# Kernel tuning notes

Measured on AMD Instinct MI355X. Metric: run time of the kernel, lower is better.

The kernel has to match this reference:

```python
import jax, jax.numpy as jnp
import numpy as np

D = 4096      # model dim
H = 32        # query heads (== kv heads; GQA path in source is buggy, default is MHA)
HD = D // H   # head_dim = 128
BASE = 10000.0


def _rope_cos_sin(S):
    # inv_freq over half the head dim, duplicated to full head_dim (standard RoPE)
    inv_freq = 1.0 / (BASE ** (jnp.arange(0, HD, 2, dtype=jnp.float32) / HD))
    t = jnp.arange(S, dtype=jnp.float32)
    freqs = jnp.outer(t, inv_freq)                      # [S, HD//2]
    cos = jnp.concatenate([jnp.cos(freqs)] * 2, axis=-1)  # [S, HD]
    sin = jnp.concatenate([jnp.sin(freqs)] * 2, axis=-1)
    return cos[None, None], sin[None, None]             # [1,1,S,HD]


def _rotate_half(x):
    x1, x2 = jnp.split(x, 2, axis=-1)
    return jnp.concatenate((-x2, x1), axis=-1)


def setup_inputs() -> dict:
    key = jax.random.key(0)
    ks = jax.random.split(key, 5)
    B, S = 2, 2048
    x = jax.random.normal(ks[0], (B, S, D), dtype=jnp.float32)
    # causal mask: 1 = attend, 0 = masked
    mask = jnp.tril(jnp.ones((S, S), dtype=bool))[None, None]  # [1,1,S,S]
    w = lambda k: jax.random.normal(k, (D, D), dtype=jnp.float32) * 0.02
    return {"x": x, "mask": mask, "Wq": w(ks[1]), "Wk": w(ks[2]), "Wv": w(ks[3]), "Wo": w(ks[4])}


def reference(x, mask, Wq, Wk, Wv, Wo):
    B, S, _ = x.shape
    scale = HD ** -0.5
    # torch nn.Linear: y = x @ W.T
    q = (x @ Wq.T).reshape(B, S, H, HD).transpose(0, 2, 1, 3)  # [B,H,S,HD]
    k = (x @ Wk.T).reshape(B, S, H, HD).transpose(0, 2, 1, 3)
    v = (x @ Wv.T).reshape(B, S, H, HD).transpose(0, 2, 1, 3)
    cos, sin = _rope_cos_sin(S)
    q = q * cos + _rotate_half(q) * sin
    k = k * cos + _rotate_half(k) * sin
    scores = jnp.einsum('bhqd,bhkd->bhqk', q, k) * scale       # [B,H,S,S]
    scores = jnp.where(mask, scores, jnp.float32(-10000.0))
    probs = jax.nn.softmax(scores, axis=-1)                    # dropout p=0.0
    ctx = jnp.einsum('bhqk,bhkd->bhqd', probs, v)
    ctx = ctx.transpose(0, 2, 1, 3).reshape(B, S, H * HD)      # [B,S,D]
    return ctx @ Wo.T
```

## Files before the change

kernel.cpp:

```cpp
#include <hip/hip_runtime.h>

typedef __bf16 bf16x8 __attribute__((ext_vector_type(8)));
typedef float  f32x4  __attribute__((ext_vector_type(4)));
typedef unsigned short ushort8v __attribute__((ext_vector_type(8)));

#define DEV __device__ __forceinline__

constexpr int Dm = 4096;
constexpr int Sq = 2048;
constexpr int Bb = 2;
constexpr int Hh = 32;
constexpr int HDd = 128;

DEV unsigned short f2bf(float f) {
  union { float f; unsigned u; } v; v.f = f;
  unsigned u = v.u;
  return (unsigned short)((u + 0x7fffu + ((u >> 16) & 1u)) >> 16);
}
DEV float bf2f(unsigned short s) {
  union { unsigned u; float f; } v; v.u = ((unsigned)s) << 16;
  return v.f;
}

__global__ __launch_bounds__(256) void cast_f32_bf16(const float* __restrict__ src,
                                                     unsigned short* __restrict__ dst,
                                                     int n8) {
  int i = blockIdx.x * 256 + threadIdx.x;
  if (i >= n8) return;
  const float4* s4 = (const float4*)src;
  float4 a = s4[2 * i], b = s4[2 * i + 1];
  ushort8v o;
  o[0] = f2bf(a.x); o[1] = f2bf(a.y); o[2] = f2bf(a.z); o[3] = f2bf(a.w);
  o[4] = f2bf(b.x); o[5] = f2bf(b.y); o[6] = f2bf(b.z); o[7] = f2bf(b.w);
  *(ushort8v*)(dst + 8 * i) = o;
}

__global__ __launch_bounds__(256) void rope_tables(float* __restrict__ cosT,
                                                   float* __restrict__ sinT) {
  int idx = blockIdx.x * 256 + threadIdx.x;
  int s = idx >> 6, i = idx & 63;
  float inv = expf(-(float)i * (9.210340371976184f / 64.0f));
  float f = (float)s * inv;
  cosT[idx] = cosf(f);
  sinT[idx] = sinf(f);
}

template <int WF32>
__global__ __launch_bounds__(256) void gemm_nt(const unsigned short* __restrict__ A,
                                               const unsigned short* __restrict__ Bw,
                                               unsigned short* __restrict__ Cb,
                                               float* __restrict__ Cf, int K) {
  constexpr int TM = 128, BK = 64;
  __shared__ unsigned short lA[TM * BK];
  __shared__ unsigned short lB[TM * BK];
  const int tid = threadIdx.x;
  const int l = tid & 63, w = tid >> 6;
  const int wm = (w >> 1) * 64, wn = (w & 1) * 64;
  const int m0 = blockIdx.x * TM, n0 = blockIdx.y * TM;
  f32x4 acc[4][4] = {};

  const int scb = (tid & 7) * 16;
  const unsigned short* Ag = A + (size_t)m0 * K;
  const unsigned short* Bg = Bw + (size_t)n0 * K;

  for (int k0 = 0; k0 < K; k0 += BK) {
    __syncthreads();
#pragma unroll
    for (int i = 0; i < 4; i++) {
      int row = (tid >> 3) + 32 * i;
      uint4 va = *(const uint4*)((const char*)Ag + ((size_t)row * K + k0) * 2 + scb);
      uint4 vb = *(const uint4*)((const char*)Bg + ((size_t)row * K + k0) * 2 + scb);
      int lo = row * 128 + (scb ^ ((row & 7) << 4));
      *(uint4*)((char*)lA + lo) = va;
      *(uint4*)((char*)lB + lo) = vb;
    }
    __syncthreads();
#pragma unroll
    for (int kc = 0; kc < 2; kc++) {
      bf16x8 af[4], bfr[4];
#pragma unroll
      for (int mi = 0; mi < 4; mi++) {
        int row = wm + mi * 16 + (l & 15);
        int cb = (kc * 64 + (l >> 4) * 16) ^ ((row & 7) << 4);
        af[mi] = *(const bf16x8*)((const char*)lA + row * 128 + cb);
      }
#pragma unroll
      for (int ni = 0; ni < 4; ni++) {
        int row = wn + ni * 16 + (l & 15);
        int cb = (kc * 64 + (l >> 4) * 16) ^ ((row & 7) << 4);
        bfr[ni] = *(const bf16x8*)((const char*)lB + row * 128 + cb);
      }
#pragma unroll
      for (int mi = 0; mi < 4; mi++)
#pragma unroll
        for (int ni = 0; ni < 4; ni++)
          acc[mi][ni] = __builtin_amdgcn_mfma_f32_16x16x32_bf16(af[mi], bfr[ni], acc[mi][ni], 0, 0, 0);
    }
  }
#pragma unroll
  for (int mi = 0; mi < 4; mi++) {
    int mrow = m0 + wm + mi * 16 + (l >> 4) * 4;
#pragma unroll
    for (int ni = 0; ni < 4; ni++) {
      int ncol = n0 + wn + ni * 16 + (l & 15);
#pragma unroll
      for (int r = 0; r < 4; r++) {
        if constexpr (WF32)
          Cf[(size_t)(mrow + r) * Dm + ncol] = acc[mi][ni][r];
        else
          Cb[(size_t)(mrow + r) * Dm + ncol] = f2bf(acc[mi][ni][r]);
      }
    }
  }
}

__global__ __launch_bounds__(256) void rope_apply(unsigned short* __restrict__ Q,
                                                  unsigned short* __restrict__ Kt,
                                                  const float* __restrict__ cosT,
                                                  const float* __restrict__ sinT) {
  int idx = blockIdx.x * 256 + threadIdx.x;
  unsigned short* P = blockIdx.y ? Kt : Q;
  int j = idx & 7;
  int h = (idx >> 3) & 31;
  int m = idx >> 8;
  int s = m & (Sq - 1);
  size_t base = (size_t)m * Dm + h * HDd + j * 8;
  ushort8v u1 = *(ushort8v*)(P + base);
  ushort8v u2 = *(ushort8v*)(P + base + 64);
  const float* cp = cosT + s * 64 + j * 8;
  const float* sp = sinT + s * 64 + j * 8;
  ushort8v o1, o2;
#pragma unroll
  for (int e = 0; e < 8; e++) {
    float c = cp[e], sn = sp[e];
    float x1 = bf2f(u1[e]), x2 = bf2f(u2[e]);
    o1[e] = f2bf(x1 * c - x2 * sn);
    o2[e] = f2bf(x2 * c + x1 * sn);
  }
  *(ushort8v*)(P + base) = o1;
  *(ushort8v*)(P + base + 64) = o2;
}

__global__ __launch_bounds__(256) void transpose_v(const unsigned short* __restrict__ V,
                                                   unsigned short* __restrict__ VT) {
  __shared__ unsigned short t[32][33];
  int bh = blockIdx.z;
  int s0 = blockIdx.x * 32, d0 = blockIdx.y * 32;
  int tx = threadIdx.x, ty = threadIdx.y;
  int b = bh >> 5, h = bh & 31;
#pragma unroll
  for (int i = 0; i < 4; i++) {
    int row = ty + i * 8;
    t[row][tx] = V[((size_t)(b * Sq + s0 + row)) * Dm + h * HDd + d0 + tx];
  }
  __syncthreads();
#pragma unroll
  for (int i = 0; i < 4; i++) {
    int row = ty + i * 8;
    VT[((size_t)bh * HDd + d0 + row) * Sq + s0 + tx] = t[tx][row];
  }
}

__global__ __launch_bounds__(256) void flash_attn(const unsigned short* __restrict__ Qg,
                                                  const unsigned short* __restrict__ Kg,
                                                  const unsigned short* __restrict__ VTg,
                                                  unsigned short* __restrict__ Ctx) {
  constexpr int QB = 64, KVB = 64, PP = 88;
  __shared__ unsigned short lK[KVB * HDd];
  __shared__ unsigned short lV[HDd * KVB];
  __shared__ unsigned short lP[4][16 * PP];
  const int tid = threadIdx.x, l = tid & 63, w = tid >> 6;
  const int q0 = blockIdx.x * QB;
  const int bh = blockIdx.y, b = bh >> 5, h = bh & 31;

  bf16x8 qf[4];
  {
    int qrow = q0 + w * 16 + (l & 15);
    const unsigned short* qp = Qg + ((size_t)(b * Sq + qrow)) * Dm + h * HDd + (l >> 4) * 8;
#pragma unroll
    for (int c = 0; c < 4; c++) qf[c] = *(const bf16x8*)(qp + c * 32);
  }

  f32x4 acc[8] = {};
  float mrun[4] = {-1e30f, -1e30f, -1e30f, -1e30f};
  float lrun[4] = {0.f, 0.f, 0.f, 0.f};
  const float scale = 0.08838834764831845f;
  const float L2E = 1.4426950408889634f;

  const int ntile = blockIdx.x + 1;
  for (int t = 0; t < ntile; t++) {
    int kv0 = t * KVB;
    __syncthreads();
#pragma unroll
    for (int i = 0; i < 4; i++) {
      int c = tid + 256 * i;
      int row = c >> 4, cb = (c & 15) * 16;
      uint4 vd = *(const uint4*)((const char*)Kg +
                                 (((size_t)(b * Sq + kv0 + row)) * Dm + h * HDd) * 2 + cb);
      *(uint4*)((char*)lK + row * 256 + (cb ^ ((row & 7) << 4))) = vd;
    }
#pragma unroll
    for (int i = 0; i < 4; i++) {
      int c = tid + 256 * i;
      int row = c >> 3, cb = (c & 7) * 16;
      uint4 vd = *(const uint4*)((const char*)VTg +
                                 (((size_t)(bh * HDd + row)) * Sq + kv0) * 2 + cb);
      *(uint4*)((char*)lV + row * 128 + (cb ^ ((row & 7) << 4))) = vd;
    }
    __syncthreads();

    f32x4 sc[4] = {};
#pragma unroll
    for (int nb = 0; nb < 4; nb++) {
      int kvr = nb * 16 + (l & 15);
#pragma unroll
      for (int c = 0; c < 4; c++) {
        int cb = (c * 64 + (l >> 4) * 16) ^ ((kvr & 7) << 4);
        bf16x8 kf = *(const bf16x8*)((const char*)lK + kvr * 256 + cb);
        sc[nb] = __builtin_amdgcn_mfma_f32_16x16x32_bf16(qf[c], kf, sc[nb], 0, 0, 0);
      }
    }

    float sv[4][4];
#pragma unroll
    for (int nb = 0; nb < 4; nb++) {
      int kvg = kv0 + nb * 16 + (l & 15);
#pragma unroll
      for (int r = 0; r < 4; r++) {
        int qg = q0 + w * 16 + (l >> 4) * 4 + r;
        float vv = sc[nb][r] * scale;
        sv[nb][r] = (kvg <= qg) ? vv : -1e30f;
      }
    }
    float rmax[4];
#pragma unroll
    for (int r = 0; r < 4; r++)
      rmax[r] = fmaxf(fmaxf(sv[0][r], sv[1][r]), fmaxf(sv[2][r], sv[3][r]));
#pragma unroll
    for (int d = 1; d < 16; d <<= 1)
#pragma unroll
      for (int r = 0; r < 4; r++) rmax[r] = fmaxf(rmax[r], __shfl_xor(rmax[r], d, 64));

    float mnew[4], alpha[4], psum[4];
#pragma unroll
    for (int r = 0; r < 4; r++) {
      mnew[r] = fmaxf(mrun[r], rmax[r]);
      alpha[r] = exp2f((mrun[r] - mnew[r]) * L2E);
      psum[r] = 0.f;
    }
    float pvv[4][4];
#pragma unroll
    for (int nb = 0; nb < 4; nb++)
#pragma unroll
      for (int r = 0; r < 4; r++) {
        float pe = exp2f((sv[nb][r] - mnew[r]) * L2E);
        pvv[nb][r] = pe;
        psum[r] += pe;
      }
#pragma unroll
    for (int d = 1; d < 16; d <<= 1)
#pragma unroll
      for (int r = 0; r < 4; r++) psum[r] += __shfl_xor(psum[r], d, 64);
#pragma unroll
    for (int r = 0; r < 4; r++) {
      lrun[r] = lrun[r] * alpha[r] + psum[r];
      mrun[r] = mnew[r];
    }
#pragma unroll
    for (int hdnb = 0; hdnb < 8; hdnb++)
#pragma unroll
      for (int r = 0; r < 4; r++) acc[hdnb][r] *= alpha[r];

    unsigned short* P = lP[w];
#pragma unroll
    for (int nb = 0; nb < 4; nb++)
#pragma unroll
      for (int r = 0; r < 4; r++)
        P[((l >> 4) * 4 + r) * PP + nb * 16 + (l & 15)] = f2bf(pvv[nb][r]);

    bf16x8 pf[2];
#pragma unroll
    for (int kc = 0; kc < 2; kc++)
      pf[kc] = *(const bf16x8*)(P + (l & 15) * PP + kc * 32 + (l >> 4) * 8);
#pragma unroll
    for (int hdnb = 0; hdnb < 8; hdnb++) {
      int hdr = hdnb * 16 + (l & 15);
#pragma unroll
      for (int kc = 0; kc < 2; kc++) {
        int cb = (kc * 64 + (l >> 4) * 16) ^ ((hdr & 7) << 4);
        bf16x8 vf = *(const bf16x8*)((const char*)lV + hdr * 128 + cb);
        acc[hdnb] = __builtin_amdgcn_mfma_f32_16x16x32_bf16(pf[kc], vf, acc[hdnb], 0, 0, 0);
      }
    }
  }

  float invl[4];
#pragma unroll
  for (int r = 0; r < 4; r++) invl[r] = 1.0f / lrun[r];
#pragma unroll
  for (int hdnb = 0; hdnb < 8; hdnb++)
#pragma unroll
    for (int r = 0; r < 4; r++) {
      size_t mrow = (size_t)(b * Sq + q0 + w * 16 + (l >> 4) * 4 + r);
      Ctx[mrow * Dm + h * HDd + hdnb * 16 + (l & 15)] = f2bf(acc[hdnb][r] * invl[r]);
    }
}

extern "C" void kernel_launch(void* const* d_in, const int* in_sizes, int n_in,
                              void* d_out, int out_size, void* d_ws, size_t ws_size,
                              hipStream_t stream) {
  (void)in_sizes; (void)n_in; (void)out_size; (void)ws_size;
  const float* x  = (const float*)d_in[0];
  const float* Wq = (const float*)d_in[2];
  const float* Wk = (const float*)d_in[3];
  const float* Wv = (const float*)d_in[4];
  const float* Wo = (const float*)d_in[5];
  float* out = (float*)d_out;

  char* p = (char*)d_ws;
  const size_t TB = (size_t)Dm * Dm * 2;
  unsigned short* xb = (unsigned short*)p; p += TB;
  unsigned short* wq = (unsigned short*)p; p += TB;
  unsigned short* wk = (unsigned short*)p; p += TB;
  unsigned short* wv = (unsigned short*)p; p += TB;
  unsigned short* wo = (unsigned short*)p; p += TB;
  unsigned short* qb = (unsigned short*)p; p += TB;
  unsigned short* kb = (unsigned short*)p; p += TB;
  unsigned short* vb = (unsigned short*)p; p += TB;
  float* cosT = (float*)p; p += (size_t)Sq * 64 * 4;
  float* sinT = (float*)p; p += (size_t)Sq * 64 * 4;
  unsigned short* vT  = xb;
  unsigned short* ctx = vb;

  const int n8 = Dm * Dm / 8;
  const int castBlocks = n8 / 256;

  cast_f32_bf16<<<castBlocks, 256, 0, stream>>>(x, xb, n8);
  cast_f32_bf16<<<castBlocks, 256, 0, stream>>>(Wq, wq, n8);
  cast_f32_bf16<<<castBlocks, 256, 0, stream>>>(Wk, wk, n8);
  cast_f32_bf16<<<castBlocks, 256, 0, stream>>>(Wv, wv, n8);
  cast_f32_bf16<<<castBlocks, 256, 0, stream>>>(Wo, wo, n8);
  rope_tables<<<512, 256, 0, stream>>>(cosT, sinT);

  dim3 gg(32, 32);
  gemm_nt<0><<<gg, 256, 0, stream>>>(xb, wq, qb, nullptr, Dm);
  gemm_nt<0><<<gg, 256, 0, stream>>>(xb, wk, kb, nullptr, Dm);
  gemm_nt<0><<<gg, 256, 0, stream>>>(xb, wv, vb, nullptr, Dm);

  rope_apply<<<dim3(4096, 2), 256, 0, stream>>>(qb, kb, cosT, sinT);
  transpose_v<<<dim3(64, 4, 64), dim3(32, 8), 0, stream>>>(vb, vT);

  flash_attn<<<dim3(Sq / 64, Bb * Hh), 256, 0, stream>>>(qb, kb, vT, ctx);

  gemm_nt<1><<<gg, 256, 0, stream>>>(ctx, wo, nullptr, out, Dm);
}
```

Before: 1.562 ms.

## Use direct global-to-LDS loads in GEMM and pipeline a larger flash-attention tile

The GEMM now loads tiles with global_load_lds straight into shared memory instead of staging them through registers, and drops the XOR swizzle. That removes register traffic but may bring back LDS bank conflicts. Flash attention moves to 128-query blocks with 8 waves, launched in reverse order so the longest causal blocks start first. It register-prefetches the next K/V tile during compute, applies the causal mask only on the last two tiles, and raises wave priority around the MFMA sections. The risks are extra barriers per tile and higher register pressure at 512 threads.

```diff
diff --git a/kernel.cpp b/kernel.cpp
--- a/kernel.cpp
+++ b/kernel.cpp
@@ -59,37 +59,39 @@
   const int m0 = blockIdx.x * TM, n0 = blockIdx.y * TM;
   f32x4 acc[4][4] = {};
 
-  const int scb = (tid & 7) * 16;
   const unsigned short* Ag = A + (size_t)m0 * K;
   const unsigned short* Bg = Bw + (size_t)n0 * K;
+  const int srow = l >> 3;
+  const int scb = (l & 7) * 16;
 
   for (int k0 = 0; k0 < K; k0 += BK) {
     __syncthreads();
 #pragma unroll
     for (int i = 0; i < 4; i++) {
-      int row = (tid >> 3) + 32 * i;
-      uint4 va = *(const uint4*)((const char*)Ag + ((size_t)row * K + k0) * 2 + scb);
-      uint4 vb = *(const uint4*)((const char*)Bg + ((size_t)row * K + k0) * 2 + scb);
-      int lo = row * 128 + (scb ^ ((row & 7) << 4));
-      *(uint4*)((char*)lA + lo) = va;
-      *(uint4*)((char*)lB + lo) = vb;
+      int row = w * 32 + i * 8 + srow;
+      __builtin_amdgcn_global_load_lds(
+          (const __attribute__((address_space(1))) void*)((const char*)Ag +
+              ((size_t)row * K + k0) * 2 + scb),
+          (__attribute__((address_space(3))) void*)(lA + (w * 4 + i) * 512),
+          16, 0, 0);
+      __builtin_amdgcn_global_load_lds(
+          (const __attribute__((address_space(1))) void*)((const char*)Bg +
+              ((size_t)row * K + k0) * 2 + scb),
+          (__attribute__((address_space(3))) void*)(lB + (w * 4 + i) * 512),
+          16, 0, 0);
     }
     __syncthreads();
 #pragma unroll
     for (int kc = 0; kc < 2; kc++) {
       bf16x8 af[4], bfr[4];
 #pragma unroll
-      for (int mi = 0; mi < 4; mi++) {
-        int row = wm + mi * 16 + (l & 15);
-        int cb = (kc * 64 + (l >> 4) * 16) ^ ((row & 7) << 4);
-        af[mi] = *(const bf16x8*)((const char*)lA + row * 128 + cb);
-      }
-#pragma unroll
-      for (int ni = 0; ni < 4; ni++) {
-        int row = wn + ni * 16 + (l & 15);
-        int cb = (kc * 64 + (l >> 4) * 16) ^ ((row & 7) << 4);
-        bfr[ni] = *(const bf16x8*)((const char*)lB + row * 128 + cb);
-      }
+      for (int mi = 0; mi < 4; mi++)
+        af[mi] = *(const bf16x8*)((const char*)lA +
+                                  (wm + mi * 16 + (l & 15)) * 128 + kc * 64 + (l >> 4) * 16);
+#pragma unroll
+      for (int ni = 0; ni < 4; ni++)
+        bfr[ni] = *(const bf16x8*)((const char*)lB +
+                                   (wn + ni * 16 + (l & 15)) * 128 + kc * 64 + (l >> 4) * 16);
 #pragma unroll
       for (int mi = 0; mi < 4; mi++)
 #pragma unroll
@@ -161,17 +163,19 @@
   }
 }
 
-__global__ __launch_bounds__(256) void flash_attn(const unsigned short* __restrict__ Qg,
+__global__ __launch_bounds__(512) void flash_attn(const unsigned short* __restrict__ Qg,
                                                   const unsigned short* __restrict__ Kg,
                                                   const unsigned short* __restrict__ VTg,
                                                   unsigned short* __restrict__ Ctx) {
-  constexpr int QB = 64, KVB = 64, PP = 88;
-  __shared__ unsigned short lK[KVB * HDd];
-  __shared__ unsigned short lV[HDd * KVB];
-  __shared__ unsigned short lP[4][16 * PP];
+  constexpr int PP = 72;
+  __shared__ unsigned short lK[64 * 128];
+  __shared__ unsigned short lV[128 * 64];
+  __shared__ unsigned short lP[8][16 * PP];
   const int tid = threadIdx.x, l = tid & 63, w = tid >> 6;
-  const int q0 = blockIdx.x * QB;
+  const int qb = gridDim.x - 1 - blockIdx.x;
+  const int q0 = qb * 128;
   const int bh = blockIdx.y, b = bh >> 5, h = bh & 31;
+  const int ntile = 2 * qb + 2;
 
   bf16x8 qf[4];
   {
@@ -187,29 +191,39 @@
   const float scale = 0.08838834764831845f;
   const float L2E = 1.4426950408889634f;
 
-  const int ntile = blockIdx.x + 1;
+  const int kr0 = tid >> 4;
+  const int kcb = (tid & 15) * 16;
+  const int vr0 = tid >> 3;
+  const int vcb = (tid & 7) * 16;
+  const char* Kbase = (const char*)Kg + ((size_t)(b * Sq) * Dm + h * HDd) * 2;
+  const char* Vbase = (const char*)VTg + ((size_t)bh * HDd) * Sq * 2;
+  uint4 kreg0, kreg1, vreg0, vreg1;
+
+  auto LOADT = [&](int kv0) {
+    kreg0 = *(const uint4*)(Kbase + (size_t)(kv0 + kr0) * (Dm * 2) + kcb);
+    kreg1 = *(const uint4*)(Kbase + (size_t)(kv0 + kr0 + 32) * (Dm * 2) + kcb);
+    vreg0 = *(const uint4*)(Vbase + (size_t)vr0 * (Sq * 2) + kv0 * 2 + vcb);
+    vreg1 = *(const uint4*)(Vbase + (size_t)(vr0 + 64) * (Sq * 2) + kv0 * 2 + vcb);
+  };
+  auto STORET = [&]() {
+    int ks = kcb ^ ((kr0 & 7) << 4);
+    int vs = vcb ^ ((vr0 & 7) << 4);
+    *(uint4*)((char*)lK + kr0 * 256 + ks) = kreg0;
+    *(uint4*)((char*)lK + (kr0 + 32) * 256 + ks) = kreg1;
+    *(uint4*)((char*)lV + vr0 * 128 + vs) = vreg0;
+    *(uint4*)((char*)lV + (vr0 + 64) * 128 + vs) = vreg1;
+  };
+
+  LOADT(0);
+  STORET();
+  __syncthreads();
+
   for (int t = 0; t < ntile; t++) {
-    int kv0 = t * KVB;
-    __syncthreads();
-#pragma unroll
-    for (int i = 0; i < 4; i++) {
-      int c = tid + 256 * i;
-      int row = c >> 4, cb = (c & 15) * 16;
-      uint4 vd = *(const uint4*)((const char*)Kg +
-                                 (((size_t)(b * Sq + kv0 + row)) * Dm + h * HDd) * 2 + cb);
-      *(uint4*)((char*)lK + row * 256 + (cb ^ ((row & 7) << 4))) = vd;
-    }
-#pragma unroll
-    for (int i = 0; i < 4; i++) {
-      int c = tid + 256 * i;
-      int row = c >> 3, cb = (c & 7) * 16;
-      uint4 vd = *(const uint4*)((const char*)VTg +
-                                 (((size_t)(bh * HDd + row)) * Sq + kv0) * 2 + cb);
-      *(uint4*)((char*)lV + row * 128 + (cb ^ ((row & 7) << 4))) = vd;
-    }
-    __syncthreads();
+    const int kv0 = t * 64;
+    if (t + 1 < ntile) LOADT((t + 1) * 64);
 
     f32x4 sc[4] = {};
+    __builtin_amdgcn_s_setprio(1);
 #pragma unroll
     for (int nb = 0; nb < 4; nb++) {
       int kvr = nb * 16 + (l & 15);
@@ -220,16 +234,21 @@
         sc[nb] = __builtin_amdgcn_mfma_f32_16x16x32_bf16(qf[c], kf, sc[nb], 0, 0, 0);
       }
     }
+    __builtin_amdgcn_s_setprio(0);
 
     float sv[4][4];
+    const bool domask = (t >= ntile - 2);
 #pragma unroll
     for (int nb = 0; nb < 4; nb++) {
       int kvg = kv0 + nb * 16 + (l & 15);
 #pragma unroll
       for (int r = 0; r < 4; r++) {
-        int qg = q0 + w * 16 + (l >> 4) * 4 + r;
         float vv = sc[nb][r] * scale;
-        sv[nb][r] = (kvg <= qg) ? vv : -1e30f;
+        if (domask) {
+          int qg = q0 + w * 16 + (l >> 4) * 4 + r;
+          vv = (kvg <= qg) ? vv : -1e30f;
+        }
+        sv[nb][r] = vv;
       }
     }
     float rmax[4];
@@ -248,13 +267,12 @@
       alpha[r] = exp2f((mrun[r] - mnew[r]) * L2E);
       psum[r] = 0.f;
     }
-    float pvv[4][4];
 #pragma unroll
     for (int nb = 0; nb < 4; nb++)
 #pragma unroll
       for (int r = 0; r < 4; r++) {
         float pe = exp2f((sv[nb][r] - mnew[r]) * L2E);
-        pvv[nb][r] = pe;
+        sv[nb][r] = pe;
         psum[r] += pe;
       }
 #pragma unroll
@@ -276,12 +294,13 @@
     for (int nb = 0; nb < 4; nb++)
 #pragma unroll
       for (int r = 0; r < 4; r++)
-        P[((l >> 4) * 4 + r) * PP + nb * 16 + (l & 15)] = f2bf(pvv[nb][r]);
+        P[((l >> 4) * 4 + r) * PP + nb * 16 + (l & 15)] = f2bf(sv[nb][r]);
 
     bf16x8 pf[2];
 #pragma unroll
     for (int kc = 0; kc < 2; kc++)
       pf[kc] = *(const bf16x8*)(P + (l & 15) * PP + kc * 32 + (l >> 4) * 8);
+    __builtin_amdgcn_s_setprio(1);
 #pragma unroll
     for (int hdnb = 0; hdnb < 8; hdnb++) {
       int hdr = hdnb * 16 + (l & 15);
@@ -292,6 +311,11 @@
         acc[hdnb] = __builtin_amdgcn_mfma_f32_16x16x32_bf16(pf[kc], vf, acc[hdnb], 0, 0, 0);
       }
     }
+    __builtin_amdgcn_s_setprio(0);
+
+    __syncthreads();
+    if (t + 1 < ntile) STORET();
+    __syncthreads();
   }
 
   float invl[4];
@@ -350,7 +374,7 @@
   rope_apply<<<dim3(4096, 2), 256, 0, stream>>>(qb, kb, cosT, sinT);
   transpose_v<<<dim3(64, 4, 64), dim3(32, 8), 0, stream>>>(vb, vT);
 
-  flash_attn<<<dim3(Sq / 64, Bb * Hh), 256, 0, stream>>>(qb, kb, vT, ctx);
+  flash_attn<<<dim3(Sq / 128, Bb * Hh), 512, 0, stream>>>(qb, kb, vT, ctx);
 
   gemm_nt<1><<<gg, 256, 0, stream>>>(ctx, wo, nullptr, out, Dm);
 }
```

Result: no change. 1.547 ms (-0.9%).
